# Performance work log

Hardware: AMD Instinct MI355X
Metric: run time of the kernel (lower is better)

The kernel has to match this reference:

```python
import jax, jax.numpy as jnp
import numpy as np

DIM, HEAD_DIM, NUM_HEAD, RP_DIM = 1024, 64, 16, 256
B, N = 2, 4096
EPS_KERNEL = 1e-4


def _orthogonal_projection(nb_rows, nb_cols, rng):
    # gaussian_orthogonal_random_matrix with scaling=0 (performer-pytorch)
    blocks = []
    full = nb_rows // nb_cols
    for _ in range(full):
        q, _ = np.linalg.qr(rng.standard_normal((nb_cols, nb_cols)))
        blocks.append(q.T)
    rem = nb_rows - full * nb_cols
    if rem > 0:
        q, _ = np.linalg.qr(rng.standard_normal((nb_cols, nb_cols)))
        blocks.append(q.T[:rem])
    mat = np.concatenate(blocks, axis=0)
    multiplier = np.linalg.norm(rng.standard_normal((nb_rows, nb_cols)), axis=1)
    return (multiplier[:, None] * mat).astype(np.float32)


def setup_inputs() -> dict:
    key = jax.random.key(0)
    ks = jax.random.split(key, 10)
    s = (1.0 / np.sqrt(DIM)).astype(np.float32)
    inp = {
        'X': jax.random.normal(ks[0], (B, N, DIM), jnp.float32),
        'mask': jnp.ones((B, N), jnp.float32),
        'W_q': jax.random.normal(ks[1], (DIM, DIM), jnp.float32) * s,
        'b_q': jnp.zeros((DIM,), jnp.float32),
        'W_k': jax.random.normal(ks[2], (DIM, DIM), jnp.float32) * s,
        'b_k': jnp.zeros((DIM,), jnp.float32),
        'W_v': jax.random.normal(ks[3], (DIM, DIM), jnp.float32) * s,
        'b_v': jnp.zeros((DIM,), jnp.float32),
        'W_ff': jax.random.normal(ks[4], (DIM, DIM), jnp.float32) * s,
        'b_ff': jnp.zeros((DIM,), jnp.float32),
        'proj': jnp.asarray(_orthogonal_projection(RP_DIM, HEAD_DIM, np.random.default_rng(0))),
    }
    return inp


def _softmax_kernel(data, proj, is_query):
    # FAVOR+ positive random features (performer-pytorch softmax_kernel)
    d = data.shape[-1]
    normalizer = d ** -0.25
    ratio = proj.shape[0] ** -0.5
    data_dash = jnp.einsum('bhnd,jd->bhnj', normalizer * data, proj)
    diag_data = jnp.sum(data * data, axis=-1, keepdims=True) * 0.5 * (normalizer ** 2)
    if is_query:
        m = jnp.max(data_dash, axis=-1, keepdims=True)
    else:
        m = jnp.max(data_dash, axis=(-1, -2), keepdims=True)
    return ratio * (jnp.exp(data_dash - diag_data - m) + EPS_KERNEL)


def _split_heads(x):
    b, n, _ = x.shape
    return x.reshape(b, n, NUM_HEAD, HEAD_DIM).transpose(0, 2, 1, 3)


def reference(X, mask, W_q, b_q, W_k, b_k, W_v, b_v, W_ff, b_ff, proj):
    Q = _split_heads(X @ W_q.T + b_q)  # [B,H,N,D]
    K = _split_heads(X @ W_k.T + b_k)
    V = _split_heads(X @ W_v.T + b_v)
    scale = HEAD_DIM ** -0.25  # 1/sqrt(sqrt(head_dim)) applied in PerformerAttention.forward
    m = mask[:, None, :, None]
    qp = _softmax_kernel(Q * scale, proj, is_query=True)   # [B,H,N,R]
    kp = _softmax_kernel(K * scale * m, proj, is_query=False)
    Vm = V * m
    # non-causal linear attention
    k_sum = jnp.sum(kp, axis=-2)                                  # [B,H,R]
    D_inv = 1.0 / jnp.einsum('bhnr,bhr->bhn', qp, k_sum)          # [B,H,N]
    context = jnp.einsum('bhnr,bhne->bhre', kp, Vm)               # [B,H,R,D]
    attn = jnp.einsum('bhre,bhnr,bhn->bhne', context, qp, D_inv)  # [B,H,N,D]
    attn = attn.transpose(0, 2, 1, 3).reshape(X.shape[0], X.shape[1], NUM_HEAD * HEAD_DIM)
    return attn @ W_ff.T + b_ff
```

## Files before the change

### kernel.cpp

```cpp
#include <hip/hip_runtime.h>
#include <math.h>

typedef unsigned short u16;
typedef short bf16x8 __attribute__((ext_vector_type(8)));
typedef float f32x4 __attribute__((ext_vector_type(4)));
typedef u16 u16x4 __attribute__((ext_vector_type(4)));

#define RATIO 0.0625f
#define EPSK 1e-4f
#define LOG2E 1.44269504f

__device__ __forceinline__ float bf2f(u16 u) {
  return __uint_as_float(((unsigned)u) << 16);
}
__device__ __forceinline__ u16 f2bf(float f) {
  unsigned x = __float_as_uint(f);
  x = x + 0x7fffu + ((x >> 16) & 1u);
  return (u16)(x >> 16);
}
__device__ __forceinline__ unsigned cvtpk(float a, float b) {
  unsigned d;
  asm("v_cvt_pk_bf16_f32 %0, %1, %2" : "=v"(d) : "v"(a), "v"(b));
  return d;
}

using as1v = __attribute__((address_space(1))) void;
using as3v = __attribute__((address_space(3))) void;
__device__ __forceinline__ void gl_lds16(const void* g, void* l) {
  __builtin_amdgcn_global_load_lds((as1v*)g, (as3v*)l, 16, 0, 0);
}

__global__ __launch_bounds__(256) void cvt_all(
    const float* __restrict__ X, const float* __restrict__ Wq, const float* __restrict__ Wk,
    const float* __restrict__ Wv, const float* __restrict__ Wff, const float* __restrict__ proj,
    u16* __restrict__ Xbf, u16* __restrict__ Wqkv, u16* __restrict__ Wffb, u16* __restrict__ Pbf) {
  long bid = blockIdx.x;
  const float* src;
  u16* dst;
  long off;
  float sc = 1.f;
  if (bid < 8192) { src = X; dst = Xbf; off = bid; }
  else if (bid < 9216) { src = Wq; dst = Wqkv; off = bid - 8192; }
  else if (bid < 10240) { src = Wk; dst = Wqkv + 1048576; off = bid - 9216; }
  else if (bid < 11264) { src = Wv; dst = Wqkv + 2097152; off = bid - 10240; }
  else if (bid < 12288) { src = Wff; dst = Wffb; off = bid - 11264; }
  else { src = proj; dst = Pbf; off = bid - 12288; sc = 0.125f; }
  long i = (off * 256 + threadIdx.x) * 4;
  f32x4 v = *(const f32x4*)(src + i);
  u16x4 o;
#pragma unroll
  for (int j = 0; j < 4; ++j) o[j] = f2bf(v[j] * sc);
  *(u16x4*)(dst + i) = o;
}

template <int EPI, int NB>
__global__ __launch_bounds__(512, 1) void gemmring(
    const u16* __restrict__ A, const u16* __restrict__ Bw,
    const float* __restrict__ bq, const float* __restrict__ bk,
    const float* __restrict__ bv, const float* __restrict__ mask,
    u16* __restrict__ Q, u16* __restrict__ Kb, u16* __restrict__ Vt,
    float* __restrict__ Of, const float* __restrict__ bff) {
  __shared__ __align__(16) u16 lds[3 * 24576];
  const int nt = 16;
  int tid = threadIdx.x;
  int l = tid & 63, w = tid >> 6;
  int wm = w >> 1, wn = w & 1;
  int lo = l & 15, hi = l >> 4;
  int bid = blockIdx.x;
  int swz = (bid & 7) * ((NB * 32) / 8) + (bid >> 3);
  long m0 = (long)(swz / NB) * 256;
  long c0 = (long)(swz % NB) * 128;
  int srow = tid >> 3;
  int sce = ((tid & 7) ^ ((tid >> 3) & 7)) * 8;
  f32x4 acc[4][4] = {};

  auto stageA = [&](int t) {
    u16* ub = (u16*)lds + (t % 3) * 24576;
    long k0 = (long)t * 64;
#pragma unroll
    for (int u = 0; u < 2; ++u)
#pragma unroll
      for (int j = 0; j < 2; ++j) {
        long row = m0 + u * 128 + j * 64 + srow;
        gl_lds16(A + row * 1024 + k0 + sce, ub + u * 8192 + j * 4096 + tid * 8);
      }
  };
  auto stageB = [&](int t) {
    u16* ub = (u16*)lds + (t % 3) * 24576 + 16384;
    long k0 = (long)t * 64;
#pragma unroll
    for (int j = 0; j < 2; ++j) {
      long row = c0 + j * 64 + srow;
      gl_lds16(Bw + row * 1024 + k0 + sce, ub + j * 4096 + tid * 8);
    }
  };

  stageA(0); stageB(0);
  stageA(1); stageB(1);

  int arb = (wm & 1) * 64;
  for (int t = 0; t < nt; ++t) {
    if (t < nt - 1) {
      asm volatile("s_waitcnt vmcnt(6)" ::: "memory");
    } else {
      asm volatile("s_waitcnt vmcnt(0)" ::: "memory");
    }
    __builtin_amdgcn_s_barrier();
    __builtin_amdgcn_sched_barrier(0);
    const u16* Au = (const u16*)lds + (t % 3) * 24576 + (wm >> 1) * 8192;
    const u16* Bu = (const u16*)lds + (t % 3) * 24576 + 16384;
    bf16x8 areg[4][2], breg[4][2];
#pragma unroll
    for (int mf = 0; mf < 4; ++mf) {
      int lrow = arb + mf * 16 + lo;
#pragma unroll
      for (int kk = 0; kk < 2; ++kk)
        areg[mf][kk] = *(const bf16x8*)(Au + lrow * 64 + ((kk * 32 + hi * 8) ^ ((lo & 7) << 3)));
    }
#pragma unroll
    for (int nf = 0; nf < 4; ++nf) {
      int lrow = wn * 64 + nf * 16 + lo;
#pragma unroll
      for (int kk = 0; kk < 2; ++kk)
        breg[nf][kk] = *(const bf16x8*)(Bu + lrow * 64 + ((kk * 32 + hi * 8) ^ ((lo & 7) << 3)));
    }
    if (t + 2 < nt) { stageA(t + 2); stageB(t + 2); }
#pragma unroll
    for (int mf = 0; mf < 4; ++mf)
#pragma unroll
      for (int nf = 0; nf < 4; ++nf)
#pragma unroll
        for (int kk = 0; kk < 2; ++kk)
          acc[mf][nf] = __builtin_amdgcn_mfma_f32_16x16x32_bf16(areg[mf][kk], breg[nf][kk],
                                                                acc[mf][nf], 0, 0, 0);
  }

  long rowb = m0 + wm * 64;
  if (EPI == 0) {
    int wsel = (int)(c0 >> 10);
    long cw = c0 & 1023;
    if (wsel < 2) {
      const float* bias = wsel ? bk : bq;
      u16* O = wsel ? Kb : Q;
#pragma unroll
      for (int mf = 0; mf < 4; ++mf)
#pragma unroll
        for (int nf = 0; nf < 4; ++nf) {
          long col = cw + wn * 64 + nf * 16 + lo;
          float bi = bias[col];
#pragma unroll
          for (int r = 0; r < 4; ++r) {
            long row = rowb + mf * 16 + hi * 4 + r;
            O[row * 1024 + col] = f2bf(acc[mf][nf][r] + bi);
          }
        }
    } else {
#pragma unroll
      for (int mf = 0; mf < 4; ++mf) {
        long t4 = rowb + mf * 16 + hi * 4;
        long b = t4 >> 12;
        long nn = t4 & 4095;
#pragma unroll
        for (int nf = 0; nf < 4; ++nf) {
          long col = cw + wn * 64 + nf * 16 + lo;
          float bi = bv[col];
          long h = col >> 6, e = col & 63;
          u16x4 pk;
#pragma unroll
          for (int r = 0; r < 4; ++r) pk[r] = f2bf((acc[mf][nf][r] + bi) * mask[t4 + r]);
          *(u16x4*)&Vt[((b * 16 + h) * 64 + e) * 4096 + nn] = pk;
        }
      }
    }
  } else {
#pragma unroll
    for (int mf = 0; mf < 4; ++mf)
#pragma unroll
      for (int nf = 0; nf < 4; ++nf) {
        long col = c0 + wn * 64 + nf * 16 + lo;
        float bi = bff[col];
#pragma unroll
        for (int r = 0; r < 4; ++r) {
          long row = rowb + mf * 16 + hi * 4 + r;
          Of[row * 1024 + col] = acc[mf][nf][r] + bi;
        }
      }
  }
}

__global__ __launch_bounds__(512) void kctx(
    const u16* __restrict__ Kg, const u16* __restrict__ Pbf,
    const u16* __restrict__ Vt, const float* __restrict__ mask,
    float* __restrict__ part, float* __restrict__ part_ks,
    float* __restrict__ part_m) {
  __shared__ __align__(16) u16 projL[256 * 64];
  __shared__ __align__(16) u16 KL[256 * 64];
  __shared__ __align__(16) u16 VL[64 * 256];
  __shared__ __align__(16) u16 kpL[256 * 64];
  __shared__ float sdiag[256];
  __shared__ float smask[256];
  int tid = threadIdx.x, l = tid & 63, wq = tid >> 6;
  int lo = l & 15, hi = l >> 4;
  int bh = blockIdx.x, ck2 = blockIdx.y;
  int b = bh >> 4, h = bh & 15;
  int rq = wq * 32;
  int rl = l >> 3;
#pragma unroll
  for (int i = 0; i < 4; ++i) {
    int c = i * 8 + wq;
    int row = c * 8 + rl;
    int sc_ = ((l & 7) * 8) ^ ((row & 7) << 3);
    gl_lds16(Pbf + (long)row * 64 + sc_, projL + c * 512);
  }
  bf16x8 ones;
#pragma unroll
  for (int e = 0; e < 8; ++e) ones[e] = (short)0x3F80;
  float Mw = -3.4e38f;
  f32x4 acc2[2][4] = {};
  f32x4 acc_ks[2] = {};
  for (int s = 0; s < 2; ++s) {
    int ck = ck2 * 2 + s;
    long tg0 = (long)b * 4096 + (long)ck * 256;
    if (s) __syncthreads();
#pragma unroll
    for (int i = 0; i < 4; ++i) {
      int c = i * 8 + wq;
      int row = c * 8 + rl;
      int sc_ = ((l & 7) * 8) ^ ((row & 7) << 3);
      gl_lds16(Kg + (tg0 + row) * 1024 + (long)h * 64 + sc_, KL + c * 512);
    }
#pragma unroll
    for (int i = 0; i < 4; ++i) {
      int c = i * 8 + wq;
      int e = 2 * c + (l >> 5);
      int sc_ = ((l & 31) * 8) ^ ((e & 7) << 3);
      gl_lds16(Vt + ((long)bh * 64 + e) * 4096 + (long)ck * 256 + sc_, VL + c * 512);
    }
    asm volatile("s_waitcnt vmcnt(0)" ::: "memory");
    __syncthreads();
    if (tid < 256) {
      float sm = 0.f;
#pragma unroll
      for (int j = 0; j < 8; ++j) {
        bf16x8 v = *(const bf16x8*)(KL + tid * 64 + ((j * 8) ^ ((tid & 7) << 3)));
#pragma unroll
        for (int e = 0; e < 8; ++e) {
          float f = bf2f((u16)v[e]);
          sm += f * f;
        }
      }
      sdiag[tid] = sm * (1.f / 128.f);
      smask[tid] = mask[tg0 + tid];
    }
    __syncthreads();
    for (int sc = 0; sc < 4; ++sc) {
      f32x4 accT[4][2] = {};
#pragma unroll
      for (int kk = 0; kk < 2; ++kk) {
        bf16x8 aK[4], bP[2];
#pragma unroll
        for (int m = 0; m < 4; ++m)
          aK[m] = *(const bf16x8*)(KL + (sc * 64 + m * 16 + lo) * 64 +
                                   ((kk * 32 + hi * 8) ^ ((lo & 7) << 3)));
#pragma unroll
        for (int nf = 0; nf < 2; ++nf)
          bP[nf] = *(const bf16x8*)(projL + (rq + nf * 16 + lo) * 64 +
                                    ((kk * 32 + hi * 8) ^ ((lo & 7) << 3)));
#pragma unroll
        for (int m = 0; m < 4; ++m)
#pragma unroll
          for (int nf = 0; nf < 2; ++nf)
            accT[m][nf] = __builtin_amdgcn_mfma_f32_16x16x32_bf16(aK[m], bP[nf], accT[m][nf], 0, 0, 0);
      }
      float mloc = -3.4e38f;
#pragma unroll
      for (int m = 0; m < 4; ++m) {
        int tb = m * 16 + hi * 4;
#pragma unroll
        for (int r = 0; r < 4; ++r) {
          float mv = smask[sc * 64 + tb + r];
#pragma unroll
          for (int nf = 0; nf < 2; ++nf) mloc = fmaxf(mloc, mv * accT[m][nf][r]);
        }
      }
#pragma unroll
      for (int sft = 1; sft < 64; sft <<= 1) mloc = fmaxf(mloc, __shfl_xor(mloc, sft, 64));
      float nM = fmaxf(Mw, mloc);
      float rs = __builtin_exp2f((Mw - nM) * LOG2E);
#pragma unroll
      for (int m = 0; m < 2; ++m)
#pragma unroll
        for (int q = 0; q < 4; ++q) {
          acc_ks[m][q] *= rs;
#pragma unroll
          for (int nf = 0; nf < 4; ++nf) acc2[m][nf][q] *= rs;
        }
      Mw = nM;
#pragma unroll
      for (int m = 0; m < 4; ++m) {
        int tb = m * 16 + hi * 4;
        float mv[4], dg[4];
#pragma unroll
        for (int r = 0; r < 4; ++r) {
          int tk = sc * 64 + tb + r;
          mv[r] = smask[tk];
          dg[r] = sdiag[tk];
        }
#pragma unroll
        for (int nf = 0; nf < 2; ++nf) {
          int rr = rq + nf * 16 + lo;
          float v[4];
#pragma unroll
          for (int r = 0; r < 4; ++r) {
            float x = mv[r] * accT[m][nf][r] - mv[r] * mv[r] * dg[r] - Mw;
            v[r] = __builtin_exp2f(x * LOG2E);
          }
          uint2 pk;
          pk.x = cvtpk(v[0], v[1]);
          pk.y = cvtpk(v[2], v[3]);
          *(uint2*)(kpL + rr * 64 + (tb ^ ((lo & 7) << 3))) = pk;
        }
      }
#pragma unroll
      for (int kk = 0; kk < 2; ++kk) {
        bf16x8 aC[2], bV[4];
#pragma unroll
        for (int m = 0; m < 2; ++m)
          aC[m] = *(const bf16x8*)(kpL + (rq + m * 16 + lo) * 64 +
                                   ((kk * 32 + hi * 8) ^ ((lo & 7) << 3)));
#pragma unroll
        for (int nf = 0; nf < 4; ++nf)
          bV[nf] = *(const bf16x8*)(VL + (nf * 16 + lo) * 256 +
                                    ((sc * 64 + kk * 32 + hi * 8) ^ ((lo & 7) << 3)));
#pragma unroll
        for (int m = 0; m < 2; ++m) {
          acc_ks[m] = __builtin_amdgcn_mfma_f32_16x16x32_bf16(aC[m], ones, acc_ks[m], 0, 0, 0);
#pragma unroll
          for (int nf = 0; nf < 4; ++nf)
            acc2[m][nf] = __builtin_amdgcn_mfma_f32_16x16x32_bf16(aC[m], bV[nf], acc2[m][nf], 0, 0, 0);
        }
      }
    }
  }
  long pb = ((long)bh * 8 + ck2) * 64;
#pragma unroll
  for (int m = 0; m < 2; ++m) {
    int r0 = rq + m * 16 + hi * 4;
#pragma unroll
    for (int nf = 0; nf < 4; ++nf) {
      int e = nf * 16 + lo;
      *(f32x4*)&part[(pb + e) * 256 + r0] = acc2[m][nf];
    }
    if (lo == 0)
      *(f32x4*)&part_ks[((long)bh * 8 + ck2) * 256 + r0] = acc_ks[m];
  }
  if (l == 0) part_m[((long)bh * 8 + ck2) * 8 + wq] = Mw;
}

__global__ __launch_bounds__(256) void ctx_reduce2(
    const float* __restrict__ part, const float* __restrict__ part_ks,
    const float* __restrict__ part_m, const u16* __restrict__ Vt,
    u16* __restrict__ ctxb) {
  __shared__ float red[256];
  int bid = blockIdx.x;
  int bh = bid / 80, j = bid % 80;
  int r = threadIdx.x;
  const float* pm = part_m + (long)bh * 64;
  float M = -3.4e38f;
#pragma unroll
  for (int i = 0; i < 64; ++i) M = fmaxf(M, pm[i]);
  int wv = r >> 5;
  float out = 0.f;
  if (j < 64) {
    float s = 0.f;
#pragma unroll
    for (int c = 0; c < 8; ++c)
      s += __builtin_exp2f((pm[c * 8 + wv] - M) * LOG2E) *
           part[(((long)bh * 8 + c) * 64 + j) * 256 + r];
    float sv = 0.f;
    const u16* vr = Vt + ((long)bh * 64 + j) * 4096 + r * 16;
#pragma unroll
    for (int q = 0; q < 2; ++q) {
      bf16x8 v = *(const bf16x8*)(vr + q * 8);
#pragma unroll
      for (int e = 0; e < 8; ++e) sv += bf2f((u16)v[e]);
    }
    red[r] = sv;
    __syncthreads();
    if (r < 32) {
      float t = 0.f;
#pragma unroll
      for (int i = 0; i < 8; ++i) t += red[r * 8 + i];
      red[r] = t;
    }
    __syncthreads();
    float svt = 0.f;
#pragma unroll
    for (int i = 0; i < 32; ++i) svt += red[i];
    out = RATIO * (s + EPSK * svt);
  } else if (j == 64) {
    float s = 0.f;
#pragma unroll
    for (int c = 0; c < 8; ++c)
      s += __builtin_exp2f((pm[c * 8 + wv] - M) * LOG2E) *
           part_ks[((long)bh * 8 + c) * 256 + r];
    out = RATIO * (s + EPSK * 4096.f);
  }
  ctxb[((long)bh * 80 + j) * 256 + r] = f2bf(out);
}

__global__ __launch_bounds__(256) void qattn(
    const u16* __restrict__ Qg, const u16* __restrict__ Pbf,
    const u16* __restrict__ ctxbg, u16* __restrict__ attn) {
  __shared__ __align__(16) u16 L[69632];
  __shared__ float sdiagq[128];
  __shared__ float sredq[4 * 128];
  u16* projL = L;
  u16* CL = L + 16384;
  u16* QL = L + 36864;
  u16* qpL = L + 36864;
  int tid = threadIdx.x, l = tid & 63, wq = tid >> 6;
  int lo = l & 15, hi = l >> 4;
  int bh = blockIdx.x;
  int b = bh >> 4, h = bh & 15;
  long tokb = (long)b * 4096 + (long)blockIdx.y * 128;
  int rq = wq * 64, tq = wq * 32;
#pragma unroll
  for (int i = 0; i < 8; ++i) {
    int c = wq * 8 + i;
    int row = c * 8 + (l >> 3);
    int sc_ = ((l & 7) * 8) ^ ((row & 7) << 3);
    gl_lds16(Pbf + (long)row * 64 + sc_, projL + c * 512);
  }
#pragma unroll
  for (int i = 0; i < 4; ++i) {
    int c = wq * 4 + i;
    int row = c * 8 + (l >> 3);
    int sc_ = ((l & 7) * 8) ^ ((row & 7) << 3);
    gl_lds16(Qg + (tokb + row) * 1024 + (long)h * 64 + sc_, QL + c * 512);
  }
#pragma unroll
  for (int i = 0; i < 10; ++i) {
    int c = wq * 10 + i;
    int j = 2 * c + (l >> 5);
    int sc_ = ((l & 31) * 8) ^ ((j & 7) << 3);
    gl_lds16(ctxbg + ((long)bh * 80 + j) * 256 + sc_, CL + c * 512);
  }
  asm volatile("s_waitcnt vmcnt(0)" ::: "memory");
  __syncthreads();
  if (tid < 128) {
    float s = 0.f;
#pragma unroll
    for (int j = 0; j < 8; ++j) {
      bf16x8 v = *(const bf16x8*)(QL + tid * 64 + ((j * 8) ^ ((tid & 7) << 3)));
#pragma unroll
      for (int e = 0; e < 8; ++e) {
        float f = bf2f((u16)v[e]);
        s += f * f;
      }
    }
    sdiagq[tid] = s * (1.f / 128.f);
  }
  f32x4 acc[4][8];
#pragma unroll
  for (int m = 0; m < 4; ++m)
#pragma unroll
    for (int nf = 0; nf < 8; ++nf) acc[m][nf] = f32x4{0.f, 0.f, 0.f, 0.f};
#pragma unroll
  for (int kk = 0; kk < 2; ++kk) {
    bf16x8 aP[4], bQ[8];
#pragma unroll
    for (int m = 0; m < 4; ++m)
      aP[m] = *(const bf16x8*)(projL + (rq + m * 16 + lo) * 64 +
                               ((kk * 32 + hi * 8) ^ ((lo & 7) << 3)));
#pragma unroll
    for (int nf = 0; nf < 8; ++nf)
      bQ[nf] = *(const bf16x8*)(QL + (nf * 16 + lo) * 64 +
                                ((kk * 32 + hi * 8) ^ ((lo & 7) << 3)));
#pragma unroll
    for (int m = 0; m < 4; ++m)
#pragma unroll
      for (int nf = 0; nf < 8; ++nf)
        acc[m][nf] = __builtin_amdgcn_mfma_f32_16x16x32_bf16(aP[m], bQ[nf], acc[m][nf], 0, 0, 0);
  }
#pragma unroll
  for (int nf = 0; nf < 8; ++nf) {
    float vm = acc[0][nf][0];
#pragma unroll
    for (int m = 0; m < 4; ++m)
#pragma unroll
      for (int r = 0; r < 4; ++r) vm = fmaxf(vm, acc[m][nf][r]);
    vm = fmaxf(vm, __shfl_xor(vm, 16, 64));
    vm = fmaxf(vm, __shfl_xor(vm, 32, 64));
    if (hi == 0) sredq[wq * 128 + nf * 16 + lo] = vm;
  }
  __syncthreads();
#pragma unroll
  for (int nf = 0; nf < 8; ++nf) {
    int tk = nf * 16 + lo;
    float rm = fmaxf(fmaxf(sredq[tk], sredq[128 + tk]),
                     fmaxf(sredq[256 + tk], sredq[384 + tk]));
    float dg = sdiagq[tk];
#pragma unroll
    for (int m = 0; m < 4; ++m) {
      int r0 = rq + m * 16 + hi * 4;
      float v[4];
#pragma unroll
      for (int r = 0; r < 4; ++r) {
        float x = acc[m][nf][r] - dg - rm;
        v[r] = RATIO * (__builtin_exp2f(x * LOG2E) + EPSK);
      }
      uint2 pk;
      pk.x = cvtpk(v[0], v[1]);
      pk.y = cvtpk(v[2], v[3]);
      *(uint2*)(qpL + tk * 256 + (r0 ^ ((lo & 7) << 3))) = pk;
    }
  }
  __syncthreads();
  f32x4 acc2[5][2];
#pragma unroll
  for (int m = 0; m < 5; ++m)
#pragma unroll
    for (int n = 0; n < 2; ++n) acc2[m][n] = f32x4{0.f, 0.f, 0.f, 0.f};
#pragma unroll
  for (int ks = 0; ks < 8; ++ks) {
    bf16x8 aC[5], bQp[2];
#pragma unroll
    for (int m = 0; m < 5; ++m)
      aC[m] = *(const bf16x8*)(CL + (m * 16 + lo) * 256 +
                               ((ks * 32 + hi * 8) ^ ((lo & 7) << 3)));
#pragma unroll
    for (int n = 0; n < 2; ++n)
      bQp[n] = *(const bf16x8*)(qpL + (tq + n * 16 + lo) * 256 +
                                ((ks * 32 + hi * 8) ^ ((lo & 7) << 3)));
#pragma unroll
    for (int m = 0; m < 5; ++m)
#pragma unroll
      for (int n = 0; n < 2; ++n)
        acc2[m][n] = __builtin_amdgcn_mfma_f32_16x16x32_bf16(aC[m], bQp[n], acc2[m][n], 0, 0, 0);
  }
#pragma unroll
  for (int n = 0; n < 2; ++n) {
    float dv = __shfl(acc2[4][n][0], lo, 64);
    float di = 1.f / dv;
    long tok = tokb + tq + n * 16 + lo;
#pragma unroll
    for (int m = 0; m < 4; ++m) {
      int j0 = m * 16 + hi * 4;
      uint2 pk;
      pk.x = cvtpk(acc2[m][n][0] * di, acc2[m][n][1] * di);
      pk.y = cvtpk(acc2[m][n][2] * di, acc2[m][n][3] * di);
      *(uint2*)&attn[tok * 1024 + (long)h * 64 + j0] = pk;
    }
  }
}

extern "C" void kernel_launch(void* const* d_in, const int* in_sizes, int n_in,
                              void* d_out, int out_size, void* d_ws, size_t ws_size,
                              hipStream_t stream) {
  const float* X = (const float*)d_in[0];
  const float* mask = (const float*)d_in[1];
  const float* Wq = (const float*)d_in[2];
  const float* bq = (const float*)d_in[3];
  const float* Wk = (const float*)d_in[4];
  const float* bk = (const float*)d_in[5];
  const float* Wv = (const float*)d_in[6];
  const float* bv = (const float*)d_in[7];
  const float* Wff = (const float*)d_in[8];
  const float* bff = (const float*)d_in[9];
  const float* proj = (const float*)d_in[10];
  float* out = (float*)d_out;

  char* p = (char*)d_ws;
  u16* Xbf = (u16*)p;   p += 16777216;
  u16* Wqkv = (u16*)p;  p += 6291456;
  u16* Wffb = (u16*)p;  p += 2097152;
  u16* Pbf = (u16*)p;   p += 32768;
  u16* Qbf = (u16*)p;   p += 16777216;
  u16* Kbf = (u16*)p;   p += 16777216;
  u16* Vt = (u16*)p;    p += 16777216;
  u16* ctxb = (u16*)p;  p += 1310720;
  float* part = (float*)p;    p += 16777216;
  float* part_ks = (float*)p; p += 262144;
  float* part_m = (float*)p;  p += 8192;
  u16* attn = Xbf;

  cvt_all<<<12304, 256, 0, stream>>>(X, Wq, Wk, Wv, Wff, proj, Xbf, Wqkv, Wffb, Pbf);
  gemmring<0, 24><<<768, 512, 0, stream>>>(Xbf, Wqkv, bq, bk, bv, mask, Qbf, Kbf, Vt, nullptr, nullptr);
  kctx<<<dim3(32, 8), 512, 0, stream>>>(Kbf, Pbf, Vt, mask, part, part_ks, part_m);
  ctx_reduce2<<<2560, 256, 0, stream>>>(part, part_ks, part_m, Vt, ctxb);
  qattn<<<dim3(32, 32), 256, 0, stream>>>(Qbf, Pbf, ctxb, attn);
  gemmring<1, 8><<<256, 512, 0, stream>>>(attn, Wffb, nullptr, nullptr, nullptr, nullptr,
                                          nullptr, nullptr, nullptr, out, bff);
}
```

Before: 162.3 us.

## Store context partials in bf16 and compute V column sums in kctx via MFMA

The kctx kernel now writes its per-chunk context partials as bf16 instead of fp32, halving the partial buffer traffic. It also computes per-chunk V column sums with an extra ones-vector MFMA in wave 0. ctx_reduce2 then reads these small partial sums instead of re-reading the whole transposed V tensor and doing a block-wide shared-memory reduction with two barriers. Rounding the partials to bf16 before the max-rescaled reduction adds some precision loss.

```diff
diff --git a/kernel.cpp b/kernel.cpp
--- a/kernel.cpp
+++ b/kernel.cpp
@@ -191,8 +191,8 @@
 __global__ __launch_bounds__(512) void kctx(
     const u16* __restrict__ Kg, const u16* __restrict__ Pbf,
     const u16* __restrict__ Vt, const float* __restrict__ mask,
-    float* __restrict__ part, float* __restrict__ part_ks,
-    float* __restrict__ part_m) {
+    u16* __restrict__ part, float* __restrict__ part_ks,
+    float* __restrict__ part_m, float* __restrict__ part_vs) {
   __shared__ __align__(16) u16 projL[256 * 64];
   __shared__ __align__(16) u16 KL[256 * 64];
   __shared__ __align__(16) u16 VL[64 * 256];
@@ -218,6 +218,7 @@
   float Mw = -3.4e38f;
   f32x4 acc2[2][4] = {};
   f32x4 acc_ks[2] = {};
+  f32x4 acc_vs[4] = {};
   for (int s = 0; s < 2; ++s) {
     int ck = ck2 * 2 + s;
     long tg0 = (long)b * 4096 + (long)ck * 256;
@@ -339,6 +340,11 @@
           for (int nf = 0; nf < 4; ++nf)
             acc2[m][nf] = __builtin_amdgcn_mfma_f32_16x16x32_bf16(aC[m], bV[nf], acc2[m][nf], 0, 0, 0);
         }
+        if (wq == 0) {
+#pragma unroll
+          for (int nf = 0; nf < 4; ++nf)
+            acc_vs[nf] = __builtin_amdgcn_mfma_f32_16x16x32_bf16(ones, bV[nf], acc_vs[nf], 0, 0, 0);
+        }
       }
     }
   }
@@ -349,19 +355,26 @@
 #pragma unroll
     for (int nf = 0; nf < 4; ++nf) {
       int e = nf * 16 + lo;
-      *(f32x4*)&part[(pb + e) * 256 + r0] = acc2[m][nf];
+      uint2 pk;
+      pk.x = cvtpk(acc2[m][nf][0], acc2[m][nf][1]);
+      pk.y = cvtpk(acc2[m][nf][2], acc2[m][nf][3]);
+      *(uint2*)&part[(pb + e) * 256 + r0] = pk;
     }
     if (lo == 0)
       *(f32x4*)&part_ks[((long)bh * 8 + ck2) * 256 + r0] = acc_ks[m];
   }
   if (l == 0) part_m[((long)bh * 8 + ck2) * 8 + wq] = Mw;
+  if (wq == 0 && hi == 0) {
+#pragma unroll
+    for (int nf = 0; nf < 4; ++nf)
+      part_vs[((long)bh * 8 + ck2) * 64 + nf * 16 + lo] = acc_vs[nf][0];
+  }
 }
 
 __global__ __launch_bounds__(256) void ctx_reduce2(
-    const float* __restrict__ part, const float* __restrict__ part_ks,
-    const float* __restrict__ part_m, const u16* __restrict__ Vt,
+    const u16* __restrict__ part, const float* __restrict__ part_ks,
+    const float* __restrict__ part_m, const float* __restrict__ part_vs,
     u16* __restrict__ ctxb) {
-  __shared__ float red[256];
   int bid = blockIdx.x;
   int bh = bid / 80, j = bid % 80;
   int r = threadIdx.x;
@@ -372,32 +385,14 @@
   int wv = r >> 5;
   float out = 0.f;
   if (j < 64) {
-    float s = 0.f;
-#pragma unroll
-    for (int c = 0; c < 8; ++c)
+    float s = 0.f, sv = 0.f;
+#pragma unroll
+    for (int c = 0; c < 8; ++c) {
       s += __builtin_exp2f((pm[c * 8 + wv] - M) * LOG2E) *
-           part[(((long)bh * 8 + c) * 64 + j) * 256 + r];
-    float sv = 0.f;
-    const u16* vr = Vt + ((long)bh * 64 + j) * 4096 + r * 16;
-#pragma unroll
-    for (int q = 0; q < 2; ++q) {
-      bf16x8 v = *(const bf16x8*)(vr + q * 8);
-#pragma unroll
-      for (int e = 0; e < 8; ++e) sv += bf2f((u16)v[e]);
-    }
-    red[r] = sv;
-    __syncthreads();
-    if (r < 32) {
-      float t = 0.f;
-#pragma unroll
-      for (int i = 0; i < 8; ++i) t += red[r * 8 + i];
-      red[r] = t;
-    }
-    __syncthreads();
-    float svt = 0.f;
-#pragma unroll
-    for (int i = 0; i < 32; ++i) svt += red[i];
-    out = RATIO * (s + EPSK * svt);
+           bf2f(part[(((long)bh * 8 + c) * 64 + j) * 256 + r]);
+      sv += part_vs[((long)bh * 8 + c) * 64 + j];
+    }
+    out = RATIO * (s + EPSK * sv);
   } else if (j == 64) {
     float s = 0.f;
 #pragma unroll
@@ -580,15 +575,16 @@
   u16* Kbf = (u16*)p;   p += 16777216;
   u16* Vt = (u16*)p;    p += 16777216;
   u16* ctxb = (u16*)p;  p += 1310720;
-  float* part = (float*)p;    p += 16777216;
+  u16* part = (u16*)p;      p += 8388608;
   float* part_ks = (float*)p; p += 262144;
   float* part_m = (float*)p;  p += 8192;
+  float* part_vs = (float*)p; p += 65536;
   u16* attn = Xbf;
 
   cvt_all<<<12304, 256, 0, stream>>>(X, Wq, Wk, Wv, Wff, proj, Xbf, Wqkv, Wffb, Pbf);
   gemmring<0, 24><<<768, 512, 0, stream>>>(Xbf, Wqkv, bq, bk, bv, mask, Qbf, Kbf, Vt, nullptr, nullptr);
-  kctx<<<dim3(32, 8), 512, 0, stream>>>(Kbf, Pbf, Vt, mask, part, part_ks, part_m);
-  ctx_reduce2<<<2560, 256, 0, stream>>>(part, part_ks, part_m, Vt, ctxb);
+  kctx<<<dim3(32, 8), 512, 0, stream>>>(Kbf, Pbf, Vt, mask, part, part_ks, part_m, part_vs);
+  ctx_reduce2<<<2560, 256, 0, stream>>>(part, part_ks, part_m, part_vs, ctxb);
   qattn<<<dim3(32, 32), 256, 0, stream>>>(Qbf, Pbf, ctxb, attn);
   gemmring<1, 8><<<256, 512, 0, stream>>>(attn, Wffb, nullptr, nullptr, nullptr, nullptr,
                                           nullptr, nullptr, nullptr, out, bff);
```

Result: faster. 158.6 us, median of 2 (-2.3%).
